# Optimization experiments

Measured on AMD Instinct MI355X. Metric: run time of the kernel, lower is better.

Reference implementation:

```python
import jax, jax.numpy as jnp
import numpy as np

RATIO = 0.8
V, F, E = 100000, 128, 3200000


def setup_inputs() -> dict:
    key = jax.random.key(0)
    k0, k1, k2, k3 = jax.random.split(key, 4)
    verts = jax.random.normal(k0, (V, F), jnp.float32)
    edges = jax.random.randint(k1, (E, 2), 0, V, dtype=jnp.int32)
    verts_idx = jnp.arange(V, dtype=jnp.int32)
    edges_idx = jnp.arange(E, dtype=jnp.int32)
    # GraphConv(in_channels=128, out=1): w0 applied to verts, w1 to summed neighbors
    w0_w = jax.random.normal(k2, (1, F), jnp.float32) * 0.05
    w0_b = jnp.zeros((1,), jnp.float32)
    w1_w = jax.random.normal(k3, (1, F), jnp.float32) * 0.05
    w1_b = jnp.zeros((1,), jnp.float32)
    return dict(verts=verts, edges=edges, verts_idx=verts_idx, edges_idx=edges_idx,
                w0_w=w0_w, w0_b=w0_b, w1_w=w1_w, w1_b=w1_b)


def graph_conv(verts, edges, w0_w, w0_b, w1_w, w1_b):
    # pytorch3d-style GraphConv: w0(v_i) + sum_{j in N(i)} w1(v_j), symmetric edges
    nv = verts.shape[0]
    vw0 = verts @ w0_w.T + w0_b            # [V,1]
    vw1 = verts @ w1_w.T + w1_b            # [V,1]
    row, col = edges[:, 0], edges[:, 1]
    nbr = jax.ops.segment_sum(vw1[col], row, num_segments=nv)
    nbr = nbr + jax.ops.segment_sum(vw1[row], col, num_segments=nv)
    return vw0 + nbr                       # [V,1]


def reference(verts, edges, verts_idx, edges_idx, w0_w, w0_b, w1_w, w1_b):
    nv = verts.shape[0]
    attn = graph_conv(verts, edges, w0_w, w0_b, w1_w, w1_b)[:, 0]  # [V]
    k = int(nv * RATIO)
    _, mask_idx = jax.lax.top_k(attn, k)
    mask_idx = jnp.sort(mask_idx)                                   # [K]
    # scatter new compacted ids into a -1 mask
    mask = jnp.full((nv,), -1, dtype=jnp.int32).at[mask_idx].set(
        jnp.arange(k, dtype=jnp.int32))
    row = mask[edges[:, 0]]
    col = mask[edges[:, 1]]
    valid = (row >= 0) & (col >= 0)
    # jit-safe compaction: stable-sort valid edges to the front, pad rest with -1
    order = jnp.argsort(~valid, stable=True)
    new_edges = jnp.stack([row, col], axis=1)[order]                # [E,2]
    valid_s = valid[order]
    new_edges = jnp.where(valid_s[:, None], new_edges, -1)
    n_edges = valid.sum()
    verts_up = verts[mask_idx] * jnp.tanh(attn[mask_idx])[:, None]  # [K,F]
    verts_idx_up = verts_idx[:k]
    edges_idx_up = jnp.where(valid_s, edges_idx[order], -1)
    return verts_up, new_edges, verts_idx_up, edges_idx_up, n_edges
```

## Files before the change

kernel.cpp:

```cpp
#include <hip/hip_runtime.h>
#include <math.h>

#define TPB 256
#define SCAN_ITEMS 4
#define SCAN_BLOCK (TPB * SCAN_ITEMS)
#define TIECAP 2048
#define HIST_BLOCKS 104
#define BW 512
#define BUCKET_BLOCKS 2048

static __device__ __forceinline__ int block_scan_excl(int v, int* lds, int& total)
{
    int lane = threadIdx.x & 63;
    int wid  = threadIdx.x >> 6;
    int x = v;
#pragma unroll
    for (int off = 1; off < 64; off <<= 1) {
        int y = __shfl_up(x, off, 64);
        if (lane >= off) x += y;
    }
    if (lane == 63) lds[wid] = x;
    __syncthreads();
    int t0 = lds[0], t1 = lds[1], t2 = lds[2], t3 = lds[3];
    int wOff = (wid > 0 ? t0 : 0) + (wid > 1 ? t1 : 0) + (wid > 2 ? t2 : 0);
    total = t0 + t1 + t2 + t3;
    __syncthreads();
    return wOff + x - v;
}

__global__ void k_init(unsigned* hist, unsigned* state, int k,
                       unsigned* cursor, int NB, int CAP)
{
    int i = threadIdx.x;
    for (int j = i; j < 1024; j += blockDim.x) hist[j] = 0u;
    if (cursor) {
        for (int j = i; j < NB; j += blockDim.x)
            cursor[j * 16] = (unsigned)(j * CAP);
    }
    if (i == 0) {
        state[0] = 0u;
        state[1] = (unsigned)k;
        state[2] = 0u;
        state[3] = 0u;
        state[4] = 0u;
    }
}

__global__ void k_dots(const float* __restrict__ verts,
                       const float* __restrict__ w0, const float* __restrict__ b0,
                       const float* __restrict__ w1, const float* __restrict__ b1,
                       long long* __restrict__ iacc, long long* __restrict__ s1q, int V)
{
    int gid  = blockIdx.x * blockDim.x + threadIdx.x;
    int v    = gid >> 6;
    int lane = gid & 63;
    if (v >= V) return;
    const float2 a  = ((const float2*)(verts + (size_t)v * 128))[lane];
    const float2 wa = ((const float2*)w0)[lane];
    const float2 wb = ((const float2*)w1)[lane];
    float p0 = a.x * wa.x + a.y * wa.y;
    float p1 = a.x * wb.x + a.y * wb.y;
#pragma unroll
    for (int off = 32; off > 0; off >>= 1) {
        p0 += __shfl_down(p0, off, 64);
        p1 += __shfl_down(p1, off, 64);
    }
    if (lane == 0) {
        double s0 = (double)p0 + (double)b0[0];
        double s1 = (double)p1 + (double)b1[0];
        iacc[v] = (long long)llrint(s0 * 1099511627776.0);
        s1q[v]  = (long long)llrint(s1 * 1099511627776.0);
    }
}

__global__ void k_scatter(const int2* __restrict__ edges, const long long* __restrict__ s1q,
                          unsigned long long* __restrict__ iacc, int E)
{
    int i = blockIdx.x * blockDim.x + threadIdx.x;
    if (i >= E) return;
    int2 e = edges[i];
    atomicAdd(&iacc[e.x], (unsigned long long)s1q[e.y]);
    atomicAdd(&iacc[e.y], (unsigned long long)s1q[e.x]);
}

__global__ void k_bucket(const int2* __restrict__ edges, const long long* __restrict__ s1q,
                         long long* __restrict__ bdata, unsigned* __restrict__ cursor,
                         int E, int NB, int CAP)
{
    __shared__ unsigned cnt[256];
    __shared__ unsigned base[256];
    const int tilesTotal = (E + 2047) / 2048;
    cnt[threadIdx.x] = 0u;
    __syncthreads();
    for (int tile = blockIdx.x; tile < tilesTotal; tile += gridDim.x) {
        int tbase = tile * 2048;
        for (int r = 0; r < 8; ++r) {
            int i = tbase + r * 256 + threadIdx.x;
            if (i < E) {
                int2 e = edges[i];
                atomicAdd(&cnt[e.x >> 9], 1u);
                atomicAdd(&cnt[e.y >> 9], 1u);
            }
        }
    }
    __syncthreads();
    if (threadIdx.x < NB) {
        unsigned c = cnt[threadIdx.x];
        base[threadIdx.x] = c ? atomicAdd(&cursor[threadIdx.x * 16], c) : 0u;
        cnt[threadIdx.x] = 0u;
    }
    __syncthreads();
    for (int tile = blockIdx.x; tile < tilesTotal; tile += gridDim.x) {
        int tbase = tile * 2048;
        for (int r = 0; r < 8; ++r) {
            int i = tbase + r * 256 + threadIdx.x;
            if (i < E) {
                int2 e = edges[i];
                long long vx = s1q[e.x], vy = s1q[e.y];
                int b0 = e.x >> 9;
                unsigned p0 = base[b0] + atomicAdd(&cnt[b0], 1u);
                if (p0 < (unsigned)(b0 + 1) * (unsigned)CAP)
                    bdata[p0] = (vy << 9) | (long long)(e.x & 511);
                int b1 = e.y >> 9;
                unsigned p1 = base[b1] + atomicAdd(&cnt[b1], 1u);
                if (p1 < (unsigned)(b1 + 1) * (unsigned)CAP)
                    bdata[p1] = (vx << 9) | (long long)(e.y & 511);
            }
        }
    }
}

__global__ void k_bucket_sum(const long long* __restrict__ bdata,
                             const unsigned* __restrict__ cursor,
                             long long* __restrict__ iacc,
                             float* __restrict__ attnf, unsigned* __restrict__ keys,
                             int V, int CAP)
{
    __shared__ unsigned long long acc[BW];
    int b = blockIdx.x;
    for (int j = threadIdx.x; j < BW; j += 256) acc[j] = 0ull;
    __syncthreads();
    unsigned n = cursor[b * 16] - (unsigned)(b * CAP);
    if (n > (unsigned)CAP) n = (unsigned)CAP;
    const long long* src = bdata + (size_t)b * CAP;
    for (unsigned i = threadIdx.x; i < n; i += 256) {
        long long p = src[i];
        atomicAdd(&acc[(int)(p & 511)], (unsigned long long)(p >> 9));
    }
    __syncthreads();
    for (int j = threadIdx.x; j < BW; j += 256) {
        int v = b * BW + j;
        if (v < V) {
            long long tot = iacc[v] + (long long)acc[j];
            float a = (float)((double)tot * 9.094947017729282379150390625e-13);
            attnf[v] = a;
            unsigned u = __float_as_uint(a);
            keys[v] = (u & 0x80000000u) ? ~u : (u | 0x80000000u);
        }
    }
}

__global__ void k_finalize(const long long* __restrict__ iacc, float* __restrict__ attnf,
                           unsigned* __restrict__ keys, int V)
{
    int i = blockIdx.x * blockDim.x + threadIdx.x;
    if (i >= V) return;
    float a = (float)((double)iacc[i] * 9.094947017729282379150390625e-13);
    attnf[i] = a;
    unsigned u = __float_as_uint(a);
    keys[i] = (u & 0x80000000u) ? ~u : (u | 0x80000000u);
}

__global__ void k_hist(const unsigned* __restrict__ keys, int V,
                       const unsigned* __restrict__ state, int shift,
                       unsigned* __restrict__ hist)
{
    __shared__ unsigned lh[256];
    lh[threadIdx.x] = 0u;
    __syncthreads();
    unsigned pref = 0u;
    if (shift != 24) pref = state[0] >> (shift + 8);
    int stride = gridDim.x * blockDim.x;
    for (int i = blockIdx.x * blockDim.x + threadIdx.x; i < V; i += stride) {
        unsigned key = keys[i];
        bool ok = (shift == 24) || ((key >> (shift + 8)) == pref);
        if (ok) atomicAdd(&lh[(key >> shift) & 255u], 1u);
    }
    __syncthreads();
    unsigned c = lh[threadIdx.x];
    if (c) atomicAdd(&hist[threadIdx.x], c);
}

__global__ void k_select(const unsigned* __restrict__ hist, int shift, unsigned* __restrict__ state)
{
    if (threadIdx.x != 0 || blockIdx.x != 0) return;
    unsigned kk = state[1];
    unsigned cum = 0;
    int j = 255;
    for (; j > 0; --j) {
        unsigned c = hist[j];
        if (cum + c >= kk) break;
        cum += c;
    }
    state[0] |= ((unsigned)j) << shift;
    state[1] = kk - cum;
    if (shift == 0) state[2] = state[0];
}

__global__ void k_tie_collect(const unsigned* __restrict__ keys, int V,
                              unsigned* __restrict__ state, int* __restrict__ selFlag,
                              int* __restrict__ tieList)
{
    int i = blockIdx.x * blockDim.x + threadIdx.x;
    if (i >= V) return;
    unsigned key = keys[i];
    unsigned T   = state[2];
    selFlag[i] = key > T ? 1 : 0;
    if (key == T) {
        unsigned p = atomicAdd(&state[3], 1u);
        if (p < TIECAP) tieList[p] = i;
    }
}

__global__ void k_tie_resolve(const unsigned* __restrict__ state,
                              const int* __restrict__ tieList, int* __restrict__ selFlag)
{
    __shared__ int s[TIECAP];
    int n  = (int)state[3];
    if (n > TIECAP) n = TIECAP;
    int kk = (int)state[1];
    int tid = threadIdx.x;
    if (kk >= n) {
        for (int i = tid; i < n; i += blockDim.x) selFlag[tieList[i]] = 1;
        return;
    }
    for (int i = tid; i < n; i += blockDim.x) s[i] = tieList[i];
    __syncthreads();
    for (int i = tid; i < n; i += blockDim.x) {
        int v = s[i];
        int r = 0;
        for (int j = 0; j < n; ++j) r += (s[j] < v);
        if (r < kk) selFlag[v] = 1;
    }
}

__global__ void k_scanA_V(const int* __restrict__ selFlag, int V, unsigned* __restrict__ bsums)
{
    __shared__ int lds[4];
    int base = blockIdx.x * SCAN_BLOCK + threadIdx.x * SCAN_ITEMS;
    int f0 = 0, f1 = 0, f2 = 0, f3 = 0;
    if (base + 3 < V) {
        int4 q = *(const int4*)(selFlag + base);
        f0 = q.x; f1 = q.y; f2 = q.z; f3 = q.w;
    } else {
        if (base     < V) f0 = selFlag[base];
        if (base + 1 < V) f1 = selFlag[base + 1];
        if (base + 2 < V) f2 = selFlag[base + 2];
        if (base + 3 < V) f3 = selFlag[base + 3];
    }
    int tot;
    block_scan_excl(f0 + f1 + f2 + f3, lds, tot);
    if (threadIdx.x == 0) bsums[blockIdx.x] = (unsigned)tot;
}

__global__ void k_scanB(unsigned* __restrict__ sums, int nb,
                        unsigned* __restrict__ totalOut, float* __restrict__ outF)
{
    __shared__ int lds[4];
    int tid = threadIdx.x;
    int running = 0;
    for (int base = 0; base < nb; base += TPB) {
        int i = base + tid;
        int v = (i < nb) ? (int)sums[i] : 0;
        int tot;
        int ex = block_scan_excl(v, lds, tot);
        if (i < nb) sums[i] = (unsigned)(ex + running);
        running += tot;
    }
    if (tid == 0) {
        if (totalOut) *totalOut = (unsigned)running;
        if (outF)     *outF    = (float)running;
    }
}

__global__ void k_scanC_V(const int* __restrict__ selFlag, int V,
                          const unsigned* __restrict__ bsums,
                          int* __restrict__ mask, int* __restrict__ selIdx,
                          const int* __restrict__ vidx_in, float* __restrict__ O2)
{
    __shared__ int lds[4];
    int base = blockIdx.x * SCAN_BLOCK + threadIdx.x * SCAN_ITEMS;
    int f[4] = {0, 0, 0, 0};
    if (base + 3 < V) {
        int4 q = *(const int4*)(selFlag + base);
        f[0] = q.x; f[1] = q.y; f[2] = q.z; f[3] = q.w;
    } else {
#pragma unroll
        for (int t = 0; t < 4; ++t)
            if (base + t < V) f[t] = selFlag[base + t];
    }
    int tot;
    int run = block_scan_excl(f[0] + f[1] + f[2] + f[3], lds, tot) + (int)bsums[blockIdx.x];
#pragma unroll
    for (int t = 0; t < 4; ++t) {
        int idx = base + t;
        if (idx < V) {
            if (f[t]) {
                mask[idx]    = run;
                selIdx[run]  = idx;
                O2[run]      = (float)vidx_in[run];
                run++;
            } else {
                mask[idx] = -1;
            }
        }
    }
}

__global__ void k_scanA_E(const int* __restrict__ edges, int E, const int* __restrict__ mask,
                          unsigned* __restrict__ bsums)
{
    __shared__ int lds[4];
    int base = blockIdx.x * SCAN_BLOCK + threadIdx.x * SCAN_ITEMS;
    int s = 0;
    if (base + 3 < E) {
        const int4* e4 = (const int4*)edges;
        int4 q0 = e4[(base >> 1)];
        int4 q1 = e4[(base >> 1) + 1];
        s += (mask[q0.x] >= 0 && mask[q0.y] >= 0);
        s += (mask[q0.z] >= 0 && mask[q0.w] >= 0);
        s += (mask[q1.x] >= 0 && mask[q1.y] >= 0);
        s += (mask[q1.z] >= 0 && mask[q1.w] >= 0);
    } else {
        for (int t = 0; t < 4; ++t) {
            int i = base + t;
            if (i < E) {
                int a = edges[2 * i], b = edges[2 * i + 1];
                s += (mask[a] >= 0 && mask[b] >= 0);
            }
        }
    }
    int tot;
    block_scan_excl(s, lds, tot);
    if (threadIdx.x == 0) bsums[blockIdx.x] = (unsigned)tot;
}

__global__ void k_scanC_E(const int* __restrict__ edges, int E, const int* __restrict__ mask,
                          const unsigned* __restrict__ bsums, const unsigned* __restrict__ state,
                          const int* __restrict__ eidx_in,
                          float* __restrict__ O1, float* __restrict__ O3)
{
    __shared__ int lds[4];
    int base = blockIdx.x * SCAN_BLOCK + threadIdx.x * SCAN_ITEMS;
    int fl[4] = {0, 0, 0, 0};
    int m0s[4], m1s[4];
    int s = 0;
#pragma unroll
    for (int t = 0; t < 4; ++t) {
        int i = base + t;
        if (i < E) {
            int2 e = ((const int2*)edges)[i];
            int m0 = mask[e.x], m1 = mask[e.y];
            m0s[t] = m0; m1s[t] = m1;
            fl[t] = (m0 >= 0 && m1 >= 0);
            s += fl[t];
        }
    }
    int tot;
    int run = block_scan_excl(s, lds, tot) + (int)bsums[blockIdx.x];
    int nValid = (int)state[4];
#pragma unroll
    for (int t = 0; t < 4; ++t) {
        int i = base + t;
        if (i < E) {
            long long pos = fl[t] ? (long long)run : (long long)nValid + (long long)(i - run);
            float2 val;
            if (fl[t]) { val.x = (float)m0s[t]; val.y = (float)m1s[t]; }
            else       { val.x = -1.0f;         val.y = -1.0f; }
            ((float2*)O1)[pos] = val;
            O3[pos] = fl[t] ? (float)eidx_in[i] : -1.0f;
            run += fl[t];
        }
    }
}

__global__ void k_verts_up(const float* __restrict__ verts, const int* __restrict__ selIdx,
                           const float* __restrict__ attnf, float* __restrict__ O0, int k)
{
    int idx = blockIdx.x * blockDim.x + threadIdx.x;
    if (idx >= k * 32) return;
    int r = idx >> 5;
    int c = idx & 31;
    int v = selIdx[r];
    float t = tanhf(attnf[v]);
    float4 x = ((const float4*)verts)[(size_t)v * 32 + c];
    x.x *= t; x.y *= t; x.z *= t; x.w *= t;
    ((float4*)O0)[(size_t)r * 32 + c] = x;
}

extern "C" void kernel_launch(void* const* d_in, const int* in_sizes, int n_in,
                              void* d_out, int out_size, void* d_ws, size_t ws_size,
                              hipStream_t stream)
{
    const float* verts = (const float*)d_in[0];
    const int*   edges = (const int*)d_in[1];
    const int*   vidx  = (const int*)d_in[2];
    const int*   eidx  = (const int*)d_in[3];
    const float* w0w   = (const float*)d_in[4];
    const float* w0b   = (const float*)d_in[5];
    const float* w1w   = (const float*)d_in[6];
    const float* w1b   = (const float*)d_in[7];

    const int V = in_sizes[2];
    const int E = in_sizes[3];
    const int F = in_sizes[0] / V;
    const int k = (int)((double)V * 0.8);

    char* p = (char*)d_ws;
    auto alloc = [&](size_t bytes) -> char* {
        char* r = p;
        p += (bytes + 255) & ~(size_t)255;
        return r;
    };
    long long* iacc   = (long long*)alloc((size_t)V * 8);
    long long* s1q    = (long long*)alloc((size_t)V * 8);
    float*     attnf  = (float*)alloc((size_t)V * 4);
    unsigned*  keys   = (unsigned*)alloc((size_t)V * 4);
    int*       selFlag= (int*)alloc((size_t)V * 4);
    int*       mask   = (int*)alloc((size_t)V * 4);
    int*       selIdx = (int*)alloc((size_t)k * 4);
    int*       tieList= (int*)alloc((size_t)TIECAP * 4);
    unsigned*  hist   = (unsigned*)alloc(1024 * 4);
    unsigned*  state  = (unsigned*)alloc(64);
    const int nbV = (V + SCAN_BLOCK - 1) / SCAN_BLOCK;
    const int nbE = (E + SCAN_BLOCK - 1) / SCAN_BLOCK;
    unsigned*  bsumsV = (unsigned*)alloc((size_t)nbV * 4);
    unsigned*  bsumsE = (unsigned*)alloc((size_t)nbE * 4);

    const int NB  = (V + BW - 1) / BW;
    long long avgc = (2LL * E * BW) / (V > 0 ? V : 1);
    const int CAP = (int)(avgc + avgc / 8 + 1024);
    unsigned*  cursor = (unsigned*)alloc(256 * 64);
    long long* bdata  = (long long*)alloc((size_t)NB * CAP * 8);
    const bool useBucket = (NB <= 256) &&
                           ((size_t)(p - (char*)d_ws) <= ws_size);

    float* out = (float*)d_out;
    float* O0 = out;
    float* O1 = O0 + (size_t)k * F;
    float* O2 = O1 + (size_t)E * 2;
    float* O3 = O2 + (size_t)k;
    float* O4 = O3 + (size_t)E;

    k_init<<<1, TPB, 0, stream>>>(hist, state, k,
                                  useBucket ? cursor : nullptr, NB, CAP);

    k_dots<<<(int)(((size_t)V * 64 + TPB - 1) / TPB), TPB, 0, stream>>>(
        verts, w0w, w0b, w1w, w1b, iacc, s1q, V);

    if (useBucket) {
        k_bucket<<<BUCKET_BLOCKS, TPB, 0, stream>>>((const int2*)edges, s1q, bdata, cursor, E, NB, CAP);
        k_bucket_sum<<<NB, TPB, 0, stream>>>(bdata, cursor, iacc, attnf, keys, V, CAP);
    } else {
        k_scatter<<<(E + TPB - 1) / TPB, TPB, 0, stream>>>(
            (const int2*)edges, s1q, (unsigned long long*)iacc, E);
        k_finalize<<<(V + TPB - 1) / TPB, TPB, 0, stream>>>(iacc, attnf, keys, V);
    }

    for (int r = 0; r < 4; ++r) {
        int shift = 24 - 8 * r;
        k_hist<<<HIST_BLOCKS, TPB, 0, stream>>>(keys, V, state, shift, hist + 256 * r);
        k_select<<<1, 64, 0, stream>>>(hist + 256 * r, shift, state);
    }

    k_tie_collect<<<(V + TPB - 1) / TPB, TPB, 0, stream>>>(keys, V, state, selFlag, tieList);
    k_tie_resolve<<<1, TPB, 0, stream>>>(state, tieList, selFlag);

    k_scanA_V<<<nbV, TPB, 0, stream>>>(selFlag, V, bsumsV);
    k_scanB<<<1, TPB, 0, stream>>>(bsumsV, nbV, nullptr, nullptr);
    k_scanC_V<<<nbV, TPB, 0, stream>>>(selFlag, V, bsumsV, mask, selIdx, vidx, O2);

    k_scanA_E<<<nbE, TPB, 0, stream>>>(edges, E, mask, bsumsE);
    k_scanB<<<1, TPB, 0, stream>>>(bsumsE, nbE, &state[4], O4);
    k_scanC_E<<<nbE, TPB, 0, stream>>>(edges, E, mask, bsumsE, state, eidx, O1, O3);

    k_verts_up<<<(k * 32 + TPB - 1) / TPB, TPB, 0, stream>>>(verts, selIdx, attnf, O0, k);
}
```

Before: 453.5 us.

## Compact bucket entries to 32-bit, fuse first histogram and scan-A into earlier kernels

The bucket pass now stores 32-bit (neighbor id, local slot) records instead of 64-bit premultiplied values, and reads the neighbor's s1q value during the bucket-sum phase. The bucket kernels use 1024-thread blocks over contiguous edge chunks with fewer blocks. The bucket sum also builds the top-byte histogram, so the first k_hist pass is skipped. Tie collection and the vertex scan-A are merged into one k_mark kernel, with tie resolution patching the block sums atomically. This cuts edge-bucket traffic and kernel launches, at the cost of random gathers of s1q in the sum phase and a V<2^17 guard on the bucket path.

```diff
diff --git a/kernel.cpp b/kernel.cpp
--- a/kernel.cpp
+++ b/kernel.cpp
@@ -7,7 +7,8 @@
 #define TIECAP 2048
 #define HIST_BLOCKS 104
 #define BW 512
-#define BUCKET_BLOCKS 2048
+#define BUCKET_BLOCKS 256
+#define BIG 1024
 
 static __device__ __forceinline__ int block_scan_excl(int v, int* lds, int& total)
 {
@@ -83,80 +84,79 @@
     atomicAdd(&iacc[e.y], (unsigned long long)s1q[e.x]);
 }
 
-__global__ void k_bucket(const int2* __restrict__ edges, const long long* __restrict__ s1q,
-                         long long* __restrict__ bdata, unsigned* __restrict__ cursor,
-                         int E, int NB, int CAP)
+__global__ void __launch_bounds__(BIG)
+k_bucket(const int2* __restrict__ edges, unsigned* __restrict__ bdata,
+         unsigned* __restrict__ cursor, int E, int NB, int CAP, int chunk)
 {
     __shared__ unsigned cnt[256];
     __shared__ unsigned base[256];
-    const int tilesTotal = (E + 2047) / 2048;
-    cnt[threadIdx.x] = 0u;
-    __syncthreads();
-    for (int tile = blockIdx.x; tile < tilesTotal; tile += gridDim.x) {
-        int tbase = tile * 2048;
-        for (int r = 0; r < 8; ++r) {
-            int i = tbase + r * 256 + threadIdx.x;
-            if (i < E) {
-                int2 e = edges[i];
-                atomicAdd(&cnt[e.x >> 9], 1u);
-                atomicAdd(&cnt[e.y >> 9], 1u);
-            }
-        }
-    }
-    __syncthreads();
-    if (threadIdx.x < NB) {
-        unsigned c = cnt[threadIdx.x];
-        base[threadIdx.x] = c ? atomicAdd(&cursor[threadIdx.x * 16], c) : 0u;
-        cnt[threadIdx.x] = 0u;
-    }
-    __syncthreads();
-    for (int tile = blockIdx.x; tile < tilesTotal; tile += gridDim.x) {
-        int tbase = tile * 2048;
-        for (int r = 0; r < 8; ++r) {
-            int i = tbase + r * 256 + threadIdx.x;
-            if (i < E) {
-                int2 e = edges[i];
-                long long vx = s1q[e.x], vy = s1q[e.y];
-                int b0 = e.x >> 9;
-                unsigned p0 = base[b0] + atomicAdd(&cnt[b0], 1u);
-                if (p0 < (unsigned)(b0 + 1) * (unsigned)CAP)
-                    bdata[p0] = (vy << 9) | (long long)(e.x & 511);
-                int b1 = e.y >> 9;
-                unsigned p1 = base[b1] + atomicAdd(&cnt[b1], 1u);
-                if (p1 < (unsigned)(b1 + 1) * (unsigned)CAP)
-                    bdata[p1] = (vx << 9) | (long long)(e.y & 511);
-            }
-        }
-    }
-}
-
-__global__ void k_bucket_sum(const long long* __restrict__ bdata,
-                             const unsigned* __restrict__ cursor,
-                             long long* __restrict__ iacc,
-                             float* __restrict__ attnf, unsigned* __restrict__ keys,
-                             int V, int CAP)
+    const int tid   = threadIdx.x;
+    const int start = blockIdx.x * chunk;
+    const int end   = min(E, start + chunk);
+    for (int j = tid; j < 256; j += BIG) cnt[j] = 0u;
+    __syncthreads();
+    for (int i = start + tid; i < end; i += BIG) {
+        int2 e = edges[i];
+        atomicAdd(&cnt[e.x >> 9], 1u);
+        atomicAdd(&cnt[e.y >> 9], 1u);
+    }
+    __syncthreads();
+    if (tid < NB) {
+        unsigned c = cnt[tid];
+        base[tid] = c ? atomicAdd(&cursor[tid * 16], c) : 0u;
+        cnt[tid] = 0u;
+    }
+    __syncthreads();
+    for (int i = start + tid; i < end; i += BIG) {
+        int2 e = edges[i];
+        int b0 = e.x >> 9;
+        unsigned p0 = base[b0] + atomicAdd(&cnt[b0], 1u);
+        if (p0 < (unsigned)(b0 + 1) * (unsigned)CAP)
+            bdata[p0] = ((unsigned)e.y << 9) | (unsigned)(e.x & 511);
+        int b1 = e.y >> 9;
+        unsigned p1 = base[b1] + atomicAdd(&cnt[b1], 1u);
+        if (p1 < (unsigned)(b1 + 1) * (unsigned)CAP)
+            bdata[p1] = ((unsigned)e.x << 9) | (unsigned)(e.y & 511);
+    }
+}
+
+__global__ void __launch_bounds__(BIG)
+k_bucket_sum(const unsigned* __restrict__ bdata, const unsigned* __restrict__ cursor,
+             const long long* __restrict__ s1q, const long long* __restrict__ iacc,
+             float* __restrict__ attnf, unsigned* __restrict__ keys,
+             unsigned* __restrict__ hist, int V, int CAP)
 {
     __shared__ unsigned long long acc[BW];
-    int b = blockIdx.x;
-    for (int j = threadIdx.x; j < BW; j += 256) acc[j] = 0ull;
+    __shared__ unsigned lh[256];
+    const int b   = blockIdx.x;
+    const int tid = threadIdx.x;
+    for (int j = tid; j < BW;  j += BIG) acc[j] = 0ull;
+    for (int j = tid; j < 256; j += BIG) lh[j] = 0u;
     __syncthreads();
     unsigned n = cursor[b * 16] - (unsigned)(b * CAP);
     if (n > (unsigned)CAP) n = (unsigned)CAP;
-    const long long* src = bdata + (size_t)b * CAP;
-    for (unsigned i = threadIdx.x; i < n; i += 256) {
-        long long p = src[i];
-        atomicAdd(&acc[(int)(p & 511)], (unsigned long long)(p >> 9));
-    }
-    __syncthreads();
-    for (int j = threadIdx.x; j < BW; j += 256) {
+    const unsigned* src = bdata + (size_t)b * CAP;
+    for (unsigned i = tid; i < n; i += BIG) {
+        unsigned p = src[i];
+        atomicAdd(&acc[p & 511u], (unsigned long long)s1q[p >> 9]);
+    }
+    __syncthreads();
+    for (int j = tid; j < BW; j += BIG) {
         int v = b * BW + j;
         if (v < V) {
             long long tot = iacc[v] + (long long)acc[j];
             float a = (float)((double)tot * 9.094947017729282379150390625e-13);
             attnf[v] = a;
             unsigned u = __float_as_uint(a);
-            keys[v] = (u & 0x80000000u) ? ~u : (u | 0x80000000u);
-        }
+            unsigned key = (u & 0x80000000u) ? ~u : (u | 0x80000000u);
+            keys[v] = key;
+            atomicAdd(&lh[key >> 24], 1u);
+        }
+    }
+    __syncthreads();
+    for (int j = tid; j < 256; j += BIG) {
+        unsigned c = lh[j];
+        if (c) atomicAdd(&hist[j], c);
     }
 }
 
@@ -207,23 +207,49 @@
     if (shift == 0) state[2] = state[0];
 }
 
-__global__ void k_tie_collect(const unsigned* __restrict__ keys, int V,
-                              unsigned* __restrict__ state, int* __restrict__ selFlag,
-                              int* __restrict__ tieList)
-{
-    int i = blockIdx.x * blockDim.x + threadIdx.x;
-    if (i >= V) return;
-    unsigned key = keys[i];
-    unsigned T   = state[2];
-    selFlag[i] = key > T ? 1 : 0;
-    if (key == T) {
-        unsigned p = atomicAdd(&state[3], 1u);
-        if (p < TIECAP) tieList[p] = i;
-    }
+__global__ void k_mark(const unsigned* __restrict__ keys, int V,
+                       unsigned* __restrict__ state, int* __restrict__ selFlag,
+                       int* __restrict__ tieList, unsigned* __restrict__ bsums)
+{
+    __shared__ int lds[4];
+    const unsigned T = state[2];
+    int base = blockIdx.x * SCAN_BLOCK + threadIdx.x * SCAN_ITEMS;
+    int f[4] = {0, 0, 0, 0};
+    unsigned kv[4];
+    bool full = (base + 3 < V);
+    if (full) {
+        uint4 q = *(const uint4*)(keys + base);
+        kv[0] = q.x; kv[1] = q.y; kv[2] = q.z; kv[3] = q.w;
+    } else {
+#pragma unroll
+        for (int t = 0; t < 4; ++t)
+            kv[t] = (base + t < V) ? keys[base + t] : 0u;
+    }
+#pragma unroll
+    for (int t = 0; t < 4; ++t) {
+        if (base + t < V) {
+            f[t] = kv[t] > T ? 1 : 0;
+            if (kv[t] == T) {
+                unsigned p = atomicAdd(&state[3], 1u);
+                if (p < TIECAP) tieList[p] = base + t;
+            }
+        }
+    }
+    if (full) {
+        *(int4*)(selFlag + base) = make_int4(f[0], f[1], f[2], f[3]);
+    } else {
+#pragma unroll
+        for (int t = 0; t < 4; ++t)
+            if (base + t < V) selFlag[base + t] = f[t];
+    }
+    int tot;
+    block_scan_excl(f[0] + f[1] + f[2] + f[3], lds, tot);
+    if (threadIdx.x == 0) bsums[blockIdx.x] = (unsigned)tot;
 }
 
 __global__ void k_tie_resolve(const unsigned* __restrict__ state,
-                              const int* __restrict__ tieList, int* __restrict__ selFlag)
+                              const int* __restrict__ tieList, int* __restrict__ selFlag,
+                              unsigned* __restrict__ bsums)
 {
     __shared__ int s[TIECAP];
     int n  = (int)state[3];
@@ -231,7 +257,11 @@
     int kk = (int)state[1];
     int tid = threadIdx.x;
     if (kk >= n) {
-        for (int i = tid; i < n; i += blockDim.x) selFlag[tieList[i]] = 1;
+        for (int i = tid; i < n; i += blockDim.x) {
+            int v = tieList[i];
+            selFlag[v] = 1;
+            atomicAdd(&bsums[v / SCAN_BLOCK], 1u);
+        }
         return;
     }
     for (int i = tid; i < n; i += blockDim.x) s[i] = tieList[i];
@@ -240,27 +270,11 @@
         int v = s[i];
         int r = 0;
         for (int j = 0; j < n; ++j) r += (s[j] < v);
-        if (r < kk) selFlag[v] = 1;
-    }
-}
-
-__global__ void k_scanA_V(const int* __restrict__ selFlag, int V, unsigned* __restrict__ bsums)
-{
-    __shared__ int lds[4];
-    int base = blockIdx.x * SCAN_BLOCK + threadIdx.x * SCAN_ITEMS;
-    int f0 = 0, f1 = 0, f2 = 0, f3 = 0;
-    if (base + 3 < V) {
-        int4 q = *(const int4*)(selFlag + base);
-        f0 = q.x; f1 = q.y; f2 = q.z; f3 = q.w;
-    } else {
-        if (base     < V) f0 = selFlag[base];
-        if (base + 1 < V) f1 = selFlag[base + 1];
-        if (base + 2 < V) f2 = selFlag[base + 2];
-        if (base + 3 < V) f3 = selFlag[base + 3];
-    }
-    int tot;
-    block_scan_excl(f0 + f1 + f2 + f3, lds, tot);
-    if (threadIdx.x == 0) bsums[blockIdx.x] = (unsigned)tot;
+        if (r < kk) {
+            selFlag[v] = 1;
+            atomicAdd(&bsums[v / SCAN_BLOCK], 1u);
+        }
+    }
 }
 
 __global__ void k_scanB(unsigned* __restrict__ sums, int nb,
@@ -441,8 +455,8 @@
     long long avgc = (2LL * E * BW) / (V > 0 ? V : 1);
     const int CAP = (int)(avgc + avgc / 8 + 1024);
     unsigned*  cursor = (unsigned*)alloc(256 * 64);
-    long long* bdata  = (long long*)alloc((size_t)NB * CAP * 8);
-    const bool useBucket = (NB <= 256) &&
+    unsigned*  bdata  = (unsigned*)alloc((size_t)NB * CAP * 4);
+    const bool useBucket = (NB <= 256) && (V < (1 << 17)) &&
                            ((size_t)(p - (char*)d_ws) <= ws_size);
 
     float* out = (float*)d_out;
@@ -459,8 +473,11 @@
         verts, w0w, w0b, w1w, w1b, iacc, s1q, V);
 
     if (useBucket) {
-        k_bucket<<<BUCKET_BLOCKS, TPB, 0, stream>>>((const int2*)edges, s1q, bdata, cursor, E, NB, CAP);
-        k_bucket_sum<<<NB, TPB, 0, stream>>>(bdata, cursor, iacc, attnf, keys, V, CAP);
+        const int chunk = (E + BUCKET_BLOCKS - 1) / BUCKET_BLOCKS;
+        k_bucket<<<BUCKET_BLOCKS, BIG, 0, stream>>>(
+            (const int2*)edges, bdata, cursor, E, NB, CAP, chunk);
+        k_bucket_sum<<<NB, BIG, 0, stream>>>(
+            bdata, cursor, s1q, iacc, attnf, keys, hist, V, CAP);
     } else {
         k_scatter<<<(E + TPB - 1) / TPB, TPB, 0, stream>>>(
             (const int2*)edges, s1q, (unsigned long long*)iacc, E);
@@ -469,14 +486,14 @@
 
     for (int r = 0; r < 4; ++r) {
         int shift = 24 - 8 * r;
-        k_hist<<<HIST_BLOCKS, TPB, 0, stream>>>(keys, V, state, shift, hist + 256 * r);
+        if (r > 0 || !useBucket)
+            k_hist<<<HIST_BLOCKS, TPB, 0, stream>>>(keys, V, state, shift, hist + 256 * r);
         k_select<<<1, 64, 0, stream>>>(hist + 256 * r, shift, state);
     }
 
-    k_tie_collect<<<(V + TPB - 1) / TPB, TPB, 0, stream>>>(keys, V, state, selFlag, tieList);
-    k_tie_resolve<<<1, TPB, 0, stream>>>(state, tieList, selFlag);
-
-    k_scanA_V<<<nbV, TPB, 0, stream>>>(selFlag, V, bsumsV);
+    k_mark<<<nbV, TPB, 0, stream>>>(keys, V, state, selFlag, tieList, bsumsV);
+    k_tie_resolve<<<1, TPB, 0, stream>>>(state, tieList, selFlag, bsumsV);
+
     k_scanB<<<1, TPB, 0, stream>>>(bsumsV, nbV, nullptr, nullptr);
     k_scanC_V<<<nbV, TPB, 0, stream>>>(selFlag, V, bsumsV, mask, selIdx, vidx, O2);
 
```

Measured after the change: 379.5 us. 16.3% less time.
